# Optimization experiments

Measured on AMD Instinct MI355X. Metric: run time of the kernel, lower is better.

## Reference

```python
import jax, jax.numpy as jnp
import numpy as np

N_SRC = 50000   # e.g. users
N_DST = 50000   # e.g. items
N = N_SRC + N_DST
E = 1_600_000   # edges (avg degree ~16)
D = 64          # in_size == out_size


def _xavier(key, shape):
    # xavier_uniform for Linear(weight shape [out, in])
    fan_out, fan_in = shape
    limit = jnp.sqrt(6.0 / (fan_in + fan_out)).astype(jnp.float32)
    return jax.random.uniform(key, shape, jnp.float32, -limit, limit)


def setup_inputs() -> dict:
    key = jax.random.key(0)
    ks = jax.random.split(key, 8)
    return {
        "src_embedding": jax.random.normal(ks[0], (N_SRC, D), jnp.float32),
        "dst_embedding": jax.random.normal(ks[1], (N_DST, D), jnp.float32),
        "norm": jax.random.uniform(ks[2], (E, 1), jnp.float32),
        "W1": _xavier(ks[3], (D, D)),
        "b1": jnp.zeros((D,), jnp.float32),
        "W2": _xavier(ks[4], (D, D)),
        "b2": jnp.zeros((D,), jnp.float32),
        "edges_src": jax.random.randint(ks[5], (E,), 0, N, dtype=jnp.int32),
        "edges_dst": jax.random.randint(ks[6], (E,), 0, N, dtype=jnp.int32),
    }


def reference(src_embedding, dst_embedding, norm, W1, b1, W2, b2,
              edges_src, edges_dst):
    # concat user/item node tables: [N, D]
    x = jnp.concatenate([src_embedding, dst_embedding], axis=0)
    xs = x[edges_src]                      # [E, D] gather (edge source nodes)
    xd = x[edges_dst]                      # [E, D] gather (edge dest nodes)
    # msgs = W1(x_src) + W2(x_src * x_dst), per edge
    msgs = (jnp.einsum('ed,od->eo', xs, W1) + b1
            + jnp.einsum('ed,od->eo', xs * xd, W2) + b2)   # [E, D]
    msgs = norm * msgs                     # per-edge scalar normalization
    # copy_e + sum: scatter-sum messages onto destination nodes
    h = jax.ops.segment_sum(msgs, edges_dst, num_segments=N)  # [N, D]
    # LeakyReLU(0.2); dropout is identity in eval / p=0
    return jnp.where(h > 0, h, 0.2 * h)
```

## Files before the change

kernel.cpp:

```cpp
#include <hip/hip_runtime.h>
#include <hip/hip_bf16.h>


#define CHUNK 4096
#define NBMAX 1024
#define BCAP  2304
#define SCAP  768
#define NSLAB 8
#define SLBSH 14

typedef __attribute__((ext_vector_type(8))) short short8v;
typedef __attribute__((ext_vector_type(4))) float f32x4;
union U4S8 { uint4 u; short8v s; };

__device__ __forceinline__ unsigned int f2bf(float f) {
    unsigned int u = __float_as_uint(f);
    u += 0x7fffu + ((u >> 16) & 1u);
    return u >> 16;
}
__device__ __forceinline__ unsigned int pkbf(float lo, float hi) {
    return (f2bf(hi) << 16) | f2bf(lo);
}

__global__ __launch_bounds__(256) void prep_init_kernel(
    const float* __restrict__ srcEmb, const float* __restrict__ dstEmb,
    unsigned int* __restrict__ xbf, int* __restrict__ gcur,
    int Ntot, int n_src, int NB)
{
    int i = blockIdx.x * 256 + threadIdx.x;
    if (i < NB) gcur[i] = i * BCAP;
    if (i >= Ntot * 32) return;
    int n = i >> 5, w = i & 31;
    const float* row = (n < n_src) ? srcEmb + (size_t)n * 64
                                   : dstEmb + (size_t)(n - n_src) * 64;
    int qlo = (int)rintf(row[w] * 128.f);
    int qhi = (int)rintf(row[w + 32] * 128.f);
    qlo = qlo > 32767 ? 32767 : (qlo < -32767 ? -32767 : qlo);
    qhi = qhi > 32767 ? 32767 : (qhi < -32767 ? -32767 : qhi);
    xbf[i] = ((unsigned int)qhi << 16) | ((unsigned int)qlo & 0xffffu);
}

__global__ __launch_bounds__(1024) void part_scatter_kernel(
    const int* __restrict__ es, const int* __restrict__ ed,
    const float* __restrict__ norm, int* __restrict__ gcur,
    uint2* __restrict__ epk, int E, int NB)
{
    __shared__ int   bcnt[NBMAX];
    __shared__ int   lstart[NBMAX];
    __shared__ int   gbase[NBMAX];
    __shared__ int   sc[NBMAX];
    __shared__ uint2 sorted[CHUNK];

    int t  = threadIdx.x;
    int e0 = blockIdx.x * CHUNK;

    bcnt[t] = 0;
    __syncthreads();

    int dreg[4];
    #pragma unroll
    for (int k = 0; k < 4; ++k) {
        int e = e0 + t + k * 1024;
        dreg[k] = (e < E) ? ed[e] : -1;
        if (dreg[k] >= 0) atomicAdd(&bcnt[dreg[k] >> 7], 1);
    }
    __syncthreads();

    int c = (t < NB) ? bcnt[t] : 0;
    sc[t] = c;
    __syncthreads();
    for (int off = 1; off < NBMAX; off <<= 1) {
        int x = 0;
        if (t >= off) x = sc[t - off];
        __syncthreads();
        if (t >= off) sc[t] += x;
        __syncthreads();
    }
    int ex = sc[t] - c;
    lstart[t] = ex;
    bcnt[t]   = ex;
    if (c > 0) gbase[t] = atomicAdd(&gcur[t], c);
    __syncthreads();

    #pragma unroll
    for (int k = 0; k < 4; ++k) {
        int e = e0 + t + k * 1024;
        if (dreg[k] >= 0) {
            unsigned int q = (unsigned int)(norm[e] * 32767.f + 0.5f);
            if (q > 32767u) q = 32767u;
            int lp = atomicAdd(&bcnt[dreg[k] >> 7], 1);
            uint2 r; r.x = (unsigned int)es[e];
            r.y = ((unsigned int)dreg[k] << 15) | q;
            sorted[lp] = r;
        }
    }
    __syncthreads();

    int total = E - e0; if (total > CHUNK) total = CHUNK;
    for (int i = t; i < total; i += 1024) {
        uint2 r = sorted[i];
        int b = (int)(r.y >> 22);
        int gpos = gbase[b] + (i - lstart[b]);
        if (gpos < (b + 1) * BCAP)
            epk[gpos] = r;
    }
}

__global__ __launch_bounds__(256) void accum_fused_kernel(
    const unsigned int* __restrict__ xbf,
    const int* __restrict__ gcur, const uint2* __restrict__ epk,
    unsigned int* __restrict__ Acat, float* __restrict__ cnt, int Ntot)
{
    __shared__ int   acc[32 * 65];
    __shared__ uint2 srt[SCAP];
    __shared__ int   sh[NSLAB];
    __shared__ int   nmyr;

    int blk = blockIdx.x;
    int b   = blk >> 2, qh = blk & 3;
    int t   = threadIdx.x;
    int base  = b * BCAP;
    int total = gcur[b] - base;
    if (total > BCAP) total = BCAP;

    for (int i = t; i < 32 * 65; i += 256) acc[i] = 0;
    if (t < NSLAB) sh[t] = 0;
    __syncthreads();

    for (int i = t; i < total; i += 256) {
        uint2 r = epk[base + i];
        int loc = (int)((r.y >> 15) & 127);
        if ((loc >> 5) == qh) atomicAdd(&sh[r.x >> SLBSH], 1);
    }
    __syncthreads();

    if (t == 0) {
        int s = 0;
        #pragma unroll
        for (int k = 0; k < NSLAB; ++k) { int c0 = sh[k]; sh[k] = s; s += c0; }
        nmyr = (s > SCAP) ? SCAP : s;
    }
    __syncthreads();

    for (int i = t; i < total; i += 256) {
        uint2 r = epk[base + i];
        int loc = (int)((r.y >> 15) & 127);
        if ((loc >> 5) == qh) {
            int pos = atomicAdd(&sh[r.x >> SLBSH], 1);
            if (pos < SCAP) srt[pos] = r;
        }
    }
    __syncthreads();

    int lane = t & 63;
    int wv   = t >> 6;
    int g    = lane >> 3;
    int sl   = lane & 7;
    int nr   = nmyr;
    int iters = (nr + 31) >> 5;

    for (int it = 0; it < iters; ++it) {
        int r = it * 32 + wv * 8 + g;
        unsigned int rx = 0u, ry = 0u;
        if (r < nr) { uint2 rc = srt[r]; rx = rc.x; ry = rc.y; }
        int wq  = (int)(ry & 0x7fffu);
        int loc = (int)((ry >> 15) & 31);
        uint4 u = *(const uint4*)(xbf + (size_t)rx * 32 + 4 * sl);
        int x0 = (int)(u.x << 16) >> 16, x4 = (int)u.x >> 16;
        int x1 = (int)(u.y << 16) >> 16, x5 = (int)u.y >> 16;
        int x2 = (int)(u.z << 16) >> 16, x6 = (int)u.z >> 16;
        int x3 = (int)(u.w << 16) >> 16, x7 = (int)u.w >> 16;
        int* a = acc + loc * 65 + 4 * sl;
        atomicAdd(a + 0,  wq * x0);
        atomicAdd(a + 1,  wq * x1);
        atomicAdd(a + 2,  wq * x2);
        atomicAdd(a + 3,  wq * x3);
        atomicAdd(a + 32, wq * x4);
        atomicAdd(a + 33, wq * x5);
        atomicAdd(a + 34, wq * x6);
        atomicAdd(a + 35, wq * x7);
        if (sl == 0) atomicAdd(acc + loc * 65 + 64, wq);
    }
    __syncthreads();

    {
        int loc = t >> 3, psl = t & 7;
        int n = b * 128 + (qh << 5) + loc;
        if (n < Ntot) {
            const float s1 = 1.f / (32767.f * 128.f);
            const int* a = acc + loc * 65 + 4 * psl;
            float ax0 = a[0]  * s1, ax1 = a[1]  * s1;
            float ax2 = a[2]  * s1, ax3 = a[3]  * s1;
            float ay0 = a[32] * s1, ay1 = a[33] * s1;
            float ay2 = a[34] * s1, ay3 = a[35] * s1;

            const float sx = 1.f / 128.f;
            uint4 xv = *(const uint4*)(xbf + (size_t)n * 32 + 4 * psl);
            float xl0 = (float)((int)(xv.x << 16) >> 16) * sx;
            float xl1 = (float)((int)(xv.y << 16) >> 16) * sx;
            float xl2 = (float)((int)(xv.z << 16) >> 16) * sx;
            float xl3 = (float)((int)(xv.w << 16) >> 16) * sx;
            float xh0 = (float)((int)xv.x >> 16) * sx;
            float xh1 = (float)((int)xv.y >> 16) * sx;
            float xh2 = (float)((int)xv.z >> 16) * sx;
            float xh3 = (float)((int)xv.w >> 16) * sx;

            uint4 w0;
            w0.x = pkbf(ax0, ax1);
            w0.y = pkbf(ax2, ax3);
            w0.z = pkbf(ay0, ay1);
            w0.w = pkbf(ay2, ay3);
            uint4 w1;
            w1.x = pkbf(ax0 * xl0, ax1 * xl1);
            w1.y = pkbf(ax2 * xl2, ax3 * xl3);
            w1.z = pkbf(ay0 * xh0, ay1 * xh1);
            w1.w = pkbf(ay2 * xh2, ay3 * xh3);
            *(uint4*)(Acat + (size_t)n * 64 + 4 * psl)      = w0;
            *(uint4*)(Acat + (size_t)n * 64 + 32 + 4 * psl) = w1;
            if (psl == 0) cnt[n] = (float)acc[loc * 65 + 64] * (1.f / 32767.f);
        }
    }
}

__global__ __launch_bounds__(256) void node_gemm_kernel(
    const unsigned int* __restrict__ Acat, const float* __restrict__ cnt,
    const float* __restrict__ W1, const float* __restrict__ b1,
    const float* __restrict__ W2, const float* __restrict__ b2,
    float* __restrict__ out, int Ntot)
{
    __shared__ unsigned int wlds[64 * 68];

    int t     = threadIdx.x;
    int lane  = t & 63;
    int wv    = t >> 6;
    int base  = blockIdx.x * 64;
    int row16 = lane & 15;
    int q     = lane >> 4;

    int arow = base + wv * 16 + row16;
    if (arow >= Ntot) arow = Ntot - 1;
    const uint4* ap = (const uint4*)(Acat + (size_t)arow * 64);
    uint4 af[4];
    #pragma unroll
    for (int s = 0; s < 4; ++s) af[s] = ap[s * 4 + q];

    for (int i = t; i < 64 * 64; i += 256) {
        int o = i >> 6, j = i & 63;
        int jj = j & 31, sl = jj >> 2, tt = jj & 3;
        int d0 = 4 * sl + ((tt & 1) << 1) + ((tt & 2) ? 32 : 0);
        const float* wsrc = (j < 32) ? W1 : W2;
        wlds[o * 68 + j] = pkbf(wsrc[o * 64 + d0], wsrc[o * 64 + d0 + 1]);
    }

    float cload[4];
    #pragma unroll
    for (int r = 0; r < 4; ++r) {
        int grow = base + wv * 16 + q * 4 + r;
        cload[r] = cnt[grow < Ntot ? grow : (Ntot - 1)];
    }
    f32x4 acc[4];
    #pragma unroll
    for (int j = 0; j < 4; ++j) {
        int col = j * 16 + row16;
        float bs = b1[col] + b2[col];
        #pragma unroll
        for (int r = 0; r < 4; ++r) acc[j][r] = cload[r] * bs;
    }
    __syncthreads();

    #pragma unroll
    for (int s = 0; s < 4; ++s) {
        U4S8 a; a.u = af[s];
        #pragma unroll
        for (int j = 0; j < 4; ++j) {
            int o = j * 16 + row16;
            U4S8 bb; bb.u = *(const uint4*)(wlds + o * 68 + s * 16 + q * 4);
            acc[j] = __builtin_amdgcn_mfma_f32_16x16x32_bf16(
                a.s, bb.s, acc[j], 0, 0, 0);
        }
    }

    #pragma unroll
    for (int r = 0; r < 4; ++r) {
        int grow = base + wv * 16 + q * 4 + r;
        if (grow < Ntot) {
            #pragma unroll
            for (int j = 0; j < 4; ++j) {
                float a = acc[j][r];
                out[(size_t)grow * 64 + j * 16 + row16] = (a > 0.f) ? a : 0.2f * a;
            }
        }
    }
}

extern "C" void kernel_launch(void* const* d_in, const int* in_sizes, int n_in,
                              void* d_out, int out_size, void* d_ws, size_t ws_size,
                              hipStream_t stream) {
    const float* srcEmb = (const float*)d_in[0];
    const float* dstEmb = (const float*)d_in[1];
    const float* norm   = (const float*)d_in[2];
    const float* W1     = (const float*)d_in[3];
    const float* b1     = (const float*)d_in[4];
    const float* W2     = (const float*)d_in[5];
    const float* b2     = (const float*)d_in[6];
    const int*   es     = (const int*)d_in[7];
    const int*   ed     = (const int*)d_in[8];

    const int n_src = in_sizes[0] / 64;
    const int n_dst = in_sizes[1] / 64;
    const int Ntot  = n_src + n_dst;
    const int E     = in_sizes[7];
    const int NB    = (Ntot + 127) >> 7;

    float* cnt      = (float*)d_ws;
    int*   gcur     = (int*)(cnt + Ntot);
    size_t off4     = (size_t)Ntot + NB;
    off4 = (off4 + 3) & ~(size_t)3;
    uint2* epk      = (uint2*)((float*)d_ws + off4);
    unsigned int* xbf = (unsigned int*)(epk + (size_t)NB * BCAP);
    unsigned int* Acat = (unsigned int*)d_out;

    prep_init_kernel<<<(Ntot * 32 + 255) / 256, 256, 0, stream>>>(
        srcEmb, dstEmb, xbf, gcur, Ntot, n_src, NB);

    part_scatter_kernel<<<(E + CHUNK - 1) / CHUNK, 1024, 0, stream>>>(
        es, ed, norm, gcur, epk, E, NB);

    accum_fused_kernel<<<NB * 4, 256, 0, stream>>>(
        xbf, gcur, epk, Acat, cnt, Ntot);

    node_gemm_kernel<<<(Ntot + 63) / 64, 256, 0, stream>>>(
        Acat, cnt, W1, b1, W2, b2, (float*)d_out, Ntot);
}
```

Baseline: 184.6 us.

## Fuse node accumulation and GEMM into one kernel via shared-memory staging

Merges the accumulate kernel and the node GEMM kernel. Each block now writes its 32 packed bf16 A-rows and counts into LDS instead of global memory, then runs the MFMA GEMM with four waves splitting rows and column halves. This removes one launch and the global round trip of the Acat and cnt intermediates. In exchange every block repacks W1/W2 into LDS, LDS use per block rises, and the srt buffer is aliased onto ubuf.

```diff
diff --git a/kernel.cpp b/kernel.cpp
--- a/kernel.cpp
+++ b/kernel.cpp
@@ -106,15 +106,21 @@
     }
 }
 
-__global__ __launch_bounds__(256) void accum_fused_kernel(
+__global__ __launch_bounds__(256) void accum_gemm_kernel(
     const unsigned int* __restrict__ xbf,
     const int* __restrict__ gcur, const uint2* __restrict__ epk,
-    unsigned int* __restrict__ Acat, float* __restrict__ cnt, int Ntot)
+    const float* __restrict__ W1, const float* __restrict__ b1,
+    const float* __restrict__ W2, const float* __restrict__ b2,
+    float* __restrict__ out, int Ntot)
 {
-    __shared__ int   acc[32 * 65];
-    __shared__ uint2 srt[SCAP];
-    __shared__ int   sh[NSLAB];
-    __shared__ int   nmyr;
+    __shared__ int          acc[32 * 65];
+    __shared__ unsigned int wlds[64 * 68];
+    __shared__ unsigned int ubuf[32 * 68];
+    __shared__ float        scn[32];
+    __shared__ int          sh[NSLAB];
+    __shared__ int          nmyr;
+
+    uint2* srt = (uint2*)ubuf;
 
     int blk = blockIdx.x;
     int b   = blk >> 2, qh = blk & 3;
@@ -125,6 +131,13 @@
 
     for (int i = t; i < 32 * 65; i += 256) acc[i] = 0;
     if (t < NSLAB) sh[t] = 0;
+    for (int i = t; i < 64 * 64; i += 256) {
+        int o = i >> 6, j = i & 63;
+        int jj = j & 31, sl = jj >> 2, tt = jj & 3;
+        int d0 = 4 * sl + ((tt & 1) << 1) + ((tt & 2) ? 32 : 0);
+        const float* wsrc = (j < 32) ? W1 : W2;
+        wlds[o * 68 + j] = pkbf(wsrc[o * 64 + d0], wsrc[o * 64 + d0 + 1]);
+    }
     __syncthreads();
 
     for (int i = t; i < total; i += 256) {
@@ -186,6 +199,7 @@
     {
         int loc = t >> 3, psl = t & 7;
         int n = b * 128 + (qh << 5) + loc;
+        uint4 w0, w1;
         if (n < Ntot) {
             const float s1 = 1.f / (32767.f * 128.f);
             const int* a = acc + loc * 65 + 4 * psl;
@@ -205,89 +219,71 @@
             float xh2 = (float)((int)xv.z >> 16) * sx;
             float xh3 = (float)((int)xv.w >> 16) * sx;
 
-            uint4 w0;
             w0.x = pkbf(ax0, ax1);
             w0.y = pkbf(ax2, ax3);
             w0.z = pkbf(ay0, ay1);
             w0.w = pkbf(ay2, ay3);
-            uint4 w1;
             w1.x = pkbf(ax0 * xl0, ax1 * xl1);
             w1.y = pkbf(ax2 * xl2, ax3 * xl3);
             w1.z = pkbf(ay0 * xh0, ay1 * xh1);
             w1.w = pkbf(ay2 * xh2, ay3 * xh3);
-            *(uint4*)(Acat + (size_t)n * 64 + 4 * psl)      = w0;
-            *(uint4*)(Acat + (size_t)n * 64 + 32 + 4 * psl) = w1;
-            if (psl == 0) cnt[n] = (float)acc[loc * 65 + 64] * (1.f / 32767.f);
-        }
-    }
-}
-
-__global__ __launch_bounds__(256) void node_gemm_kernel(
-    const unsigned int* __restrict__ Acat, const float* __restrict__ cnt,
-    const float* __restrict__ W1, const float* __restrict__ b1,
-    const float* __restrict__ W2, const float* __restrict__ b2,
-    float* __restrict__ out, int Ntot)
-{
-    __shared__ unsigned int wlds[64 * 68];
-
-    int t     = threadIdx.x;
-    int lane  = t & 63;
-    int wv    = t >> 6;
-    int base  = blockIdx.x * 64;
-    int row16 = lane & 15;
-    int q     = lane >> 4;
-
-    int arow = base + wv * 16 + row16;
-    if (arow >= Ntot) arow = Ntot - 1;
-    const uint4* ap = (const uint4*)(Acat + (size_t)arow * 64);
-    uint4 af[4];
-    #pragma unroll
-    for (int s = 0; s < 4; ++s) af[s] = ap[s * 4 + q];
-
-    for (int i = t; i < 64 * 64; i += 256) {
-        int o = i >> 6, j = i & 63;
-        int jj = j & 31, sl = jj >> 2, tt = jj & 3;
-        int d0 = 4 * sl + ((tt & 1) << 1) + ((tt & 2) ? 32 : 0);
-        const float* wsrc = (j < 32) ? W1 : W2;
-        wlds[o * 68 + j] = pkbf(wsrc[o * 64 + d0], wsrc[o * 64 + d0 + 1]);
-    }
-
-    float cload[4];
-    #pragma unroll
-    for (int r = 0; r < 4; ++r) {
-        int grow = base + wv * 16 + q * 4 + r;
-        cload[r] = cnt[grow < Ntot ? grow : (Ntot - 1)];
-    }
-    f32x4 acc[4];
-    #pragma unroll
-    for (int j = 0; j < 4; ++j) {
-        int col = j * 16 + row16;
-        float bs = b1[col] + b2[col];
-        #pragma unroll
-        for (int r = 0; r < 4; ++r) acc[j][r] = cload[r] * bs;
-    }
-    __syncthreads();
-
-    #pragma unroll
-    for (int s = 0; s < 4; ++s) {
-        U4S8 a; a.u = af[s];
-        #pragma unroll
-        for (int j = 0; j < 4; ++j) {
-            int o = j * 16 + row16;
-            U4S8 bb; bb.u = *(const uint4*)(wlds + o * 68 + s * 16 + q * 4);
-            acc[j] = __builtin_amdgcn_mfma_f32_16x16x32_bf16(
-                a.s, bb.s, acc[j], 0, 0, 0);
-        }
-    }
-
-    #pragma unroll
-    for (int r = 0; r < 4; ++r) {
-        int grow = base + wv * 16 + q * 4 + r;
-        if (grow < Ntot) {
+            if (psl == 0) scn[loc] = (float)acc[loc * 65 + 64] * (1.f / 32767.f);
+        } else {
+            w0.x = w0.y = w0.z = w0.w = 0u;
+            w1.x = w1.y = w1.z = w1.w = 0u;
+            if (psl == 0) scn[loc] = 0.f;
+        }
+        *(uint4*)(ubuf + loc * 68 + 4 * psl)      = w0;
+        *(uint4*)(ubuf + loc * 68 + 32 + 4 * psl) = w1;
+    }
+    __syncthreads();
+
+    {
+        int rt = wv & 1, cp = wv >> 1;
+        int row16 = lane & 15;
+        int q     = lane >> 4;
+        int arow  = rt * 16 + row16;
+
+        uint4 af[4];
+        #pragma unroll
+        for (int s = 0; s < 4; ++s)
+            af[s] = *(const uint4*)(ubuf + arow * 68 + s * 16 + q * 4);
+
+        float cload[4];
+        #pragma unroll
+        for (int r = 0; r < 4; ++r) cload[r] = scn[rt * 16 + q * 4 + r];
+
+        f32x4 acc2[2];
+        #pragma unroll
+        for (int j = 0; j < 2; ++j) {
+            int col = cp * 32 + j * 16 + row16;
+            float bs = b1[col] + b2[col];
             #pragma unroll
-            for (int j = 0; j < 4; ++j) {
-                float a = acc[j][r];
-                out[(size_t)grow * 64 + j * 16 + row16] = (a > 0.f) ? a : 0.2f * a;
+            for (int r = 0; r < 4; ++r) acc2[j][r] = cload[r] * bs;
+        }
+
+        #pragma unroll
+        for (int s = 0; s < 4; ++s) {
+            U4S8 a; a.u = af[s];
+            #pragma unroll
+            for (int j = 0; j < 2; ++j) {
+                int o = cp * 32 + j * 16 + row16;
+                U4S8 bb; bb.u = *(const uint4*)(wlds + o * 68 + s * 16 + q * 4);
+                acc2[j] = __builtin_amdgcn_mfma_f32_16x16x32_bf16(
+                    a.s, bb.s, acc2[j], 0, 0, 0);
+            }
+        }
+
+        #pragma unroll
+        for (int r = 0; r < 4; ++r) {
+            int grow = b * 128 + (qh << 5) + rt * 16 + q * 4 + r;
+            if (grow < Ntot) {
+                #pragma unroll
+                for (int j = 0; j < 2; ++j) {
+                    float a = acc2[j][r];
+                    out[(size_t)grow * 64 + cp * 32 + j * 16 + row16] =
+                        (a > 0.f) ? a : 0.2f * a;
+                }
             }
         }
     }
@@ -312,13 +308,11 @@
     const int E     = in_sizes[7];
     const int NB    = (Ntot + 127) >> 7;
 
-    float* cnt      = (float*)d_ws;
-    int*   gcur     = (int*)(cnt + Ntot);
-    size_t off4     = (size_t)Ntot + NB;
+    int*   gcur     = (int*)d_ws;
+    size_t off4     = (size_t)NB;
     off4 = (off4 + 3) & ~(size_t)3;
-    uint2* epk      = (uint2*)((float*)d_ws + off4);
+    uint2* epk      = (uint2*)((int*)d_ws + off4);
     unsigned int* xbf = (unsigned int*)(epk + (size_t)NB * BCAP);
-    unsigned int* Acat = (unsigned int*)d_out;
 
     prep_init_kernel<<<(Ntot * 32 + 255) / 256, 256, 0, stream>>>(
         srcEmb, dstEmb, xbf, gcur, Ntot, n_src, NB);
@@ -326,9 +320,6 @@
     part_scatter_kernel<<<(E + CHUNK - 1) / CHUNK, 1024, 0, stream>>>(
         es, ed, norm, gcur, epk, E, NB);
 
-    accum_fused_kernel<<<NB * 4, 256, 0, stream>>>(
-        xbf, gcur, epk, Acat, cnt, Ntot);
-
-    node_gemm_kernel<<<(Ntot + 63) / 64, 256, 0, stream>>>(
-        Acat, cnt, W1, b1, W2, b2, (float*)d_out, Ntot);
-}
+    accum_gemm_kernel<<<NB * 4, 256, 0, stream>>>(
+        xbf, gcur, epk, W1, b1, W2, b2, (float*)d_out, Ntot);
+}
```

After: 203.6 us. 1.1x slower.
